# Performance work log

Measured on AMD Instinct MI355X. Metric: run time of the kernel, lower is better.

The kernel has to match this reference:

```python
import jax, jax.numpy as jnp
import numpy as np

N_NODES = 100000
DIM = 64
E_RAND = 1600000
NEG_SLOPE = 0.2


def setup_inputs() -> dict:
    key = jax.random.key(0)
    k = jax.random.split(key, 10)
    x = jax.random.normal(k[0], (N_NODES, DIM), dtype=jnp.float32)
    # random edges with src != dst, then append self-loops (PyG add_self_loops=True)
    src = jax.random.randint(k[1], (E_RAND,), 0, N_NODES)
    off = jax.random.randint(k[2], (E_RAND,), 1, N_NODES)
    dst = (src + off) % N_NODES
    loops = jnp.arange(N_NODES)
    edge_index = jnp.stack([jnp.concatenate([src, loops]),
                            jnp.concatenate([dst, loops])]).astype(jnp.int32)
    s = 1.0 / np.sqrt(DIM)  # ~glorot scale
    W_l = jax.random.normal(k[3], (DIM, DIM), dtype=jnp.float32) * s
    b_l = jnp.zeros((DIM,), dtype=jnp.float32)
    W_r = jax.random.normal(k[4], (DIM, DIM), dtype=jnp.float32) * s
    b_r = jnp.zeros((DIM,), dtype=jnp.float32)
    att = jax.random.normal(k[5], (DIM,), dtype=jnp.float32) * s
    bias = jnp.zeros((DIM,), dtype=jnp.float32)
    return {"x": x, "edge_index": edge_index, "W_l": W_l, "b_l": b_l,
            "W_r": W_r, "b_r": b_r, "att": att, "bias": bias}


def _gatv2_conv(x, src, dst, W_l, b_l, W_r, b_r, att, bias):
    # GATv2Conv, heads=1, concat=True, share_weights=False
    x_l = x @ W_l + b_l          # source/message transform  [N, D]
    x_r = x @ W_r + b_r          # target transform          [N, D]
    h = jax.nn.leaky_relu(x_l[src] + x_r[dst], NEG_SLOPE)  # [E, D]
    e = h @ att                  # per-edge score            [E]
    # scatter-softmax over incoming edges of each destination node
    m = jax.ops.segment_max(e, dst, num_segments=N_NODES)
    ex = jnp.exp(e - m[dst])
    denom = jax.ops.segment_sum(ex, dst, num_segments=N_NODES)
    alpha = ex / denom[dst]      # [E]
    out = jax.ops.segment_sum(alpha[:, None] * x_l[src], dst, num_segments=N_NODES)
    return out + bias


def reference(x, edge_index, W_l, b_l, W_r, b_r, att, bias):
    src, dst = edge_index[0], edge_index[1]
    h = _gatv2_conv(x, src, dst, W_l, b_l, W_r, b_r, att, bias)
    h = _gatv2_conv(h, src, dst, W_l, b_l, W_r, b_r, att, bias)
    return x + h  # residual=True
```

## Files before the change

kernel.cpp:

```cpp
#include <hip/hip_runtime.h>
#include <hip/hip_fp16.h>

#define DIMN 64
#define LROWS 128
#define XPAD 132
#define BK 256
#define NBMAX 512
#define P1E 8192
#define CAPB 6144

typedef _Float16 f16x2 __attribute__((ext_vector_type(2)));

__device__ __forceinline__ f16x2 asH2(unsigned u) {
  f16x2 r;
  __builtin_memcpy(&r, &u, 4);
  return r;
}
__device__ __forceinline__ unsigned asU(f16x2 h) {
  unsigned u;
  __builtin_memcpy(&u, &h, 4);
  return u;
}
__device__ __forceinline__ float4 cvt4u(uint2 u) {
  f16x2 a = asH2(u.x), b = asH2(u.y);
  return make_float4((float)a[0], (float)a[1], (float)b[0], (float)b[1]);
}
__device__ __forceinline__ uint2 pack4(float4 v) {
  f16x2 a = {(_Float16)v.x, (_Float16)v.y};
  f16x2 b = {(_Float16)v.z, (_Float16)v.w};
  uint2 u;
  u.x = asU(a);
  u.y = asU(b);
  return u;
}

template <bool IN_HALF>
__device__ __forceinline__ void linear_body(
    const void* __restrict__ xin,
    const float* __restrict__ Wl, const float* __restrict__ bl,
    const float* __restrict__ Wr, const float* __restrict__ br,
    __half* __restrict__ xlh, __half* __restrict__ xrh, int N, int bid,
    float* sWl, float* sWr, float* sxT)
{
  const float4* Wl4 = (const float4*)Wl;
  const float4* Wr4 = (const float4*)Wr;
  float4* sWl4 = (float4*)sWl;
  float4* sWr4 = (float4*)sWr;
  for (int i = threadIdx.x; i < DIMN * DIMN / 4; i += 256) {
    sWl4[i] = Wl4[i];
    sWr4[i] = Wr4[i];
  }
  int base = bid * LROWS;
  int nrows = min(LROWS, N - base);
  for (int i = threadIdx.x; i < LROWS * (DIMN / 4); i += 256) {
    int r = i >> 4;
    int k4 = (i & 15) * 4;
    float4 v = make_float4(0.f, 0.f, 0.f, 0.f);
    if (r < nrows) {
      if constexpr (IN_HALF)
        v = cvt4u(((const uint2*)xin)[(size_t)base * 16 + i]);
      else
        v = ((const float4*)xin)[(size_t)base * 16 + i];
    }
    sxT[(k4 + 0) * XPAD + r] = v.x;
    sxT[(k4 + 1) * XPAD + r] = v.y;
    sxT[(k4 + 2) * XPAD + r] = v.z;
    sxT[(k4 + 3) * XPAD + r] = v.w;
  }
  __syncthreads();

  int sub = threadIdx.x & 15;
  int dg = sub * 4;
  int rg = (threadIdx.x >> 4) * 8;
  float4 bl4 = *(const float4*)(bl + dg);
  float4 br4 = *(const float4*)(br + dg);
  float4 al[8], ar[8];
#pragma unroll
  for (int j = 0; j < 8; ++j) { al[j] = bl4; ar[j] = br4; }
#pragma unroll 2
  for (int k = 0; k < DIMN; ++k) {
    float4 wl = *(const float4*)(sWl + k * DIMN + dg);
    float4 wr = *(const float4*)(sWr + k * DIMN + dg);
    const float* xp = sxT + k * XPAD + rg;
    float4 xa = *(const float4*)(xp);
    float4 xb = *(const float4*)(xp + 4);
    float xs0 = xa.x, xs1 = xa.y, xs2 = xa.z, xs3 = xa.w;
    float xs4 = xb.x, xs5 = xb.y, xs6 = xb.z, xs7 = xb.w;
#define FMA_ROW(J, XV)                                              \
    al[J].x = fmaf(XV, wl.x, al[J].x);                              \
    al[J].y = fmaf(XV, wl.y, al[J].y);                              \
    al[J].z = fmaf(XV, wl.z, al[J].z);                              \
    al[J].w = fmaf(XV, wl.w, al[J].w);                              \
    ar[J].x = fmaf(XV, wr.x, ar[J].x);                              \
    ar[J].y = fmaf(XV, wr.y, ar[J].y);                              \
    ar[J].z = fmaf(XV, wr.z, ar[J].z);                              \
    ar[J].w = fmaf(XV, wr.w, ar[J].w);
    FMA_ROW(0, xs0) FMA_ROW(1, xs1) FMA_ROW(2, xs2) FMA_ROW(3, xs3)
    FMA_ROW(4, xs4) FMA_ROW(5, xs5) FMA_ROW(6, xs6) FMA_ROW(7, xs7)
#undef FMA_ROW
  }
#pragma unroll
  for (int j = 0; j < 8; ++j) {
    int r = base + rg + j;
    if (r < N) {
      ((uint2*)xlh)[(unsigned)r * 16u + sub] = pack4(al[j]);
      ((uint2*)xrh)[(unsigned)r * 16u + sub] = pack4(ar[j]);
    }
  }
}

__device__ __forceinline__ void p1_body(
    const int* __restrict__ src, const int* __restrict__ dst,
    int* __restrict__ bucketCnt, int* __restrict__ packed, int E,
    int bid, int* cnt, int* basea)
{
  for (int i = threadIdx.x; i < NBMAX; i += 256) cnt[i] = 0;
  __syncthreads();
  int e0 = bid * P1E;
  int e1 = min(e0 + P1E, E);
  for (int e = e0 + threadIdx.x; e < e1; e += 256)
    atomicAdd(&cnt[dst[e] >> 8], 1);
  __syncthreads();
  for (int b = threadIdx.x; b < NBMAX; b += 256) {
    int c = cnt[b];
    basea[b] = (c > 0) ? atomicAdd(&bucketCnt[b], c) : 0;
    cnt[b] = 0;
  }
  __syncthreads();
  for (int e = e0 + threadIdx.x; e < e1; e += 256) {
    int d = dst[e];
    int b = d >> 8;
    int pos = basea[b] + atomicAdd(&cnt[b], 1);
    if (pos < CAPB)
      packed[(size_t)b * CAPB + pos] = ((d & 255) << 24) | src[e];
  }
}

__global__ __launch_bounds__(256) void k_lin_p1(
    const float* __restrict__ x,
    const float* __restrict__ Wl, const float* __restrict__ bl,
    const float* __restrict__ Wr, const float* __restrict__ br,
    __half* __restrict__ xlh, __half* __restrict__ xrh, int N,
    const int* __restrict__ src, const int* __restrict__ dst,
    int* __restrict__ bucketCnt, int* __restrict__ packed, int E, int p1Grid)
{
  __shared__ __align__(16) float sWl[DIMN * DIMN];
  __shared__ __align__(16) float sWr[DIMN * DIMN];
  __shared__ __align__(16) float sxT[DIMN * XPAD];
  int bid = blockIdx.x;
  if (bid < p1Grid) {
    p1_body(src, dst, bucketCnt, packed, E, bid, (int*)sWl, (int*)sWr);
    return;
  }
  linear_body<false>(x, Wl, bl, Wr, br, xlh, xrh, N, bid - p1Grid,
                     sWl, sWr, sxT);
}

__global__ __launch_bounds__(256) void k_linear2(
    const __half* __restrict__ xin,
    const float* __restrict__ Wl, const float* __restrict__ bl,
    const float* __restrict__ Wr, const float* __restrict__ br,
    __half* __restrict__ xlh, __half* __restrict__ xrh, int N)
{
  __shared__ __align__(16) float sWl[DIMN * DIMN];
  __shared__ __align__(16) float sWr[DIMN * DIMN];
  __shared__ __align__(16) float sxT[DIMN * XPAD];
  linear_body<true>(xin, Wl, bl, Wr, br, xlh, xrh, N, blockIdx.x,
                    sWl, sWr, sxT);
}

__global__ __launch_bounds__(256) void k_p2(
    const int* __restrict__ packed, const int* __restrict__ bucketCnt,
    int* __restrict__ rowptr, int* __restrict__ deg,
    int* __restrict__ csr_src, int N)
{
  __shared__ int hist[BK];
  __shared__ int off[BK];
  __shared__ int cur[BK];
  int b = blockIdx.x;
  int t = threadIdx.x;
  int node0 = b * BK;
  int nn = min(BK, N - node0);
  hist[t] = 0;
  cur[t] = 0;
  __syncthreads();
  int cntB = min(bucketCnt[b], CAPB);
  const int* pk = packed + (size_t)b * CAPB;
  for (int i = t; i < cntB; i += 256)
    atomicAdd(&hist[(unsigned)pk[i] >> 24], 1);
  __syncthreads();
  int sz = (t < nn) ? ((hist[t] + 7) & ~7) : 0;
  off[t] = sz;
  __syncthreads();
  for (int s = 1; s < BK; s <<= 1) {
    int add = (t >= s) ? off[t - s] : 0;
    __syncthreads();
    off[t] += add;
    __syncthreads();
  }
  int aStart = (t == 0) ? 0 : off[t - 1];
  __syncthreads();
  off[t] = aStart;
  if (t < nn) {
    rowptr[node0 + t] = b * CAPB + aStart;
    deg[node0 + t] = hist[t];
  }
  __syncthreads();
  int* cb = csr_src + (size_t)b * CAPB;
  if (t < nn) {
    for (int z = aStart + hist[t]; z < aStart + sz; ++z) cb[z] = 0;
    if (t == nn - 1) {
      int e = aStart + sz;
      for (int k = 0; k < 24; ++k)
        if (e + k < CAPB) cb[e + k] = 0;
    }
  }
  __syncthreads();
  for (int i = t; i < cntB; i += 256) {
    int v = pk[i];
    int dl = (unsigned)v >> 24;
    int pos = off[dl] + atomicAdd(&cur[dl], 1);
    cb[pos] = (v & 0xFFFFFF) << 3;
  }
}

template <bool OUT_HALF>
__global__ __launch_bounds__(256) void k_node(
    const __half* __restrict__ xlh, const __half* __restrict__ xrh,
    const int* __restrict__ rowptr, const int* __restrict__ deg,
    const int* __restrict__ csr_src,
    const float* __restrict__ att, const float* __restrict__ bias,
    const float* __restrict__ resid, void* __restrict__ out, int N)
{
  int node = blockIdx.x * 4 + (threadIdx.x >> 6);
  int lane = threadIdx.x & 63;
  if (node >= N) return;
  int g = lane >> 3;
  int sub = lane & 7;
  int beg = rowptr[node];
  int cnt = deg[node];
  const int* cs = csr_src + beg;
  const uint4* xp = (const uint4*)xlh;

  uint4 ur = ((const uint4*)xrh)[(unsigned)node * 8u + sub];
  f16x2 xr0 = asH2(ur.x), xr1 = asH2(ur.y);
  f16x2 xr2 = asH2(ur.z), xr3 = asH2(ur.w);
  float4 ata = ((const float4*)att)[2 * sub];
  float4 atb = ((const float4*)att)[2 * sub + 1];
  f16x2 at0 = {(_Float16)ata.x, (_Float16)ata.y};
  f16x2 at1 = {(_Float16)ata.z, (_Float16)ata.w};
  f16x2 at2 = {(_Float16)atb.x, (_Float16)atb.y};
  f16x2 at3 = {(_Float16)atb.z, (_Float16)atb.w};
  const f16x2 k02 = {(_Float16)0.2f, (_Float16)0.2f};

  float den = 0.f;
  float4 ac0 = make_float4(0.f, 0.f, 0.f, 0.f);
  float4 ac1 = make_float4(0.f, 0.f, 0.f, 0.f);

  int niter = (cnt + 7) >> 3;
  uint4 ra = xp[(unsigned)cs[g] + sub];
  int q1 = (1 < niter) ? cs[8 + g] : 0;
  uint4 rb = xp[(unsigned)q1 + sub];
  int q2 = (2 < niter) ? cs[16 + g] : 0;

#define BODY(F, P_EXTRA)                                            \
    f16x2 x0 = asH2(F.x), x1 = asH2(F.y);                           \
    f16x2 x2 = asH2(F.z), x3 = asH2(F.w);                           \
    f16x2 s0 = x0 + xr0, s1 = x1 + xr1;                             \
    f16x2 s2 = x2 + xr2, s3 = x3 + xr3;                             \
    s0 = __builtin_elementwise_max(s0, s0 * k02);                   \
    s1 = __builtin_elementwise_max(s1, s1 * k02);                   \
    s2 = __builtin_elementwise_max(s2, s2 * k02);                   \
    s3 = __builtin_elementwise_max(s3, s3 * k02);                   \
    float wa = __builtin_amdgcn_fdot2(at0, s0, 0.f, false);         \
    float wb = __builtin_amdgcn_fdot2(at2, s2, 0.f, false);         \
    wa = __builtin_amdgcn_fdot2(at1, s1, wa, false);                \
    wb = __builtin_amdgcn_fdot2(at3, s3, wb, false);                \
    float w = wa + wb;                                              \
    w += __shfl_xor(w, 1);                                          \
    w += __shfl_xor(w, 2);                                          \
    w += __shfl_xor(w, 4);                                          \
    P_EXTRA                                                         \
    float p = __expf(w);                                            \
    den += p;                                                       \
    ac0.x = fmaf(p, (float)x0[0], ac0.x);                           \
    ac0.y = fmaf(p, (float)x0[1], ac0.y);                           \
    ac0.z = fmaf(p, (float)x1[0], ac0.z);                           \
    ac0.w = fmaf(p, (float)x1[1], ac0.w);                           \
    ac1.x = fmaf(p, (float)x2[0], ac1.x);                           \
    ac1.y = fmaf(p, (float)x2[1], ac1.y);                           \
    ac1.z = fmaf(p, (float)x3[0], ac1.z);                           \
    ac1.w = fmaf(p, (float)x3[1], ac1.w);

  int i = 0;
  for (; i < niter - 1; ++i) {
    uint4 rc = ra;
    if (i + 2 < niter) rc = xp[(unsigned)q2 + sub];
    int q3 = 0;
    if (i + 3 < niter) q3 = cs[((i + 3) << 3) + g];
    BODY(ra, )
    ra = rb; rb = rc; q2 = q3;
  }
  {
    BODY(ra, w = ((i << 3) + g < cnt) ? w : -INFINITY;)
  }
#undef BODY

  den += __shfl_xor(den, 8);
  den += __shfl_xor(den, 16);
  den += __shfl_xor(den, 32);
  bool l1 = (g & 1) == 0;
  float k0 = l1 ? ac0.x : ac1.x;
  float k1 = l1 ? ac0.y : ac1.y;
  float k2 = l1 ? ac0.z : ac1.z;
  float k3 = l1 ? ac0.w : ac1.w;
  k0 += __shfl_xor(l1 ? ac1.x : ac0.x, 8);
  k1 += __shfl_xor(l1 ? ac1.y : ac0.y, 8);
  k2 += __shfl_xor(l1 ? ac1.z : ac0.z, 8);
  k3 += __shfl_xor(l1 ? ac1.w : ac0.w, 8);
  bool l2 = (g & 2) == 0;
  float t0 = l2 ? k0 : k2;
  float t1 = l2 ? k1 : k3;
  t0 += __shfl_xor(l2 ? k2 : k0, 16);
  t1 += __shfl_xor(l2 ? k3 : k1, 16);
  bool l3 = (g & 4) == 0;
  float uk = l3 ? t0 : t1;
  uk += __shfl_xor(l3 ? t1 : t0, 32);
  int d = 8 * sub + (((g & 1) << 2) | (g & 2) | ((g & 4) >> 2));
  float inv = 1.0f / den;
  float o = fmaf(uk, inv, bias[d]);
  if constexpr (OUT_HALF) {
    ((_Float16*)out)[(unsigned)node * 64u + d] = (_Float16)o;
  } else {
    if (resid) o += resid[(unsigned)node * 64u + d];
    ((float*)out)[(unsigned)node * 64u + d] = o;
  }
}

extern "C" void kernel_launch(void* const* d_in, const int* in_sizes, int n_in,
                              void* d_out, int out_size, void* d_ws, size_t ws_size,
                              hipStream_t stream) {
  const float* x    = (const float*)d_in[0];
  const int*   ei   = (const int*)d_in[1];
  const float* W_l  = (const float*)d_in[2];
  const float* b_l  = (const float*)d_in[3];
  const float* W_r  = (const float*)d_in[4];
  const float* b_r  = (const float*)d_in[5];
  const float* att  = (const float*)d_in[6];
  const float* bias = (const float*)d_in[7];
  float* out = (float*)d_out;

  const int N = in_sizes[0] / DIMN;
  const int E = in_sizes[1] / 2;
  const int* src = ei;
  const int* dst = ei + E;
  const int nb = (N + BK - 1) / BK;

  __half* xlh = (__half*)d_ws;
  __half* xrh = xlh + (size_t)N * DIMN;
  __half* hh  = xrh + (size_t)N * DIMN;
  int* deg       = (int*)(hh + (size_t)N * DIMN);
  int* rowptr    = deg + N;
  int* bucketCnt = rowptr + N;
  int* csr_src   = bucketCnt + NBMAX;
  int* packed    = (int*)hh;

  const int linGrid  = (N + LROWS - 1) / LROWS;
  const int nodeGrid = (N + 3) / 4;
  const int p1Grid   = (E + P1E - 1) / P1E;

  hipMemsetAsync(bucketCnt, 0, (size_t)NBMAX * 4, stream);
  k_lin_p1<<<p1Grid + linGrid, 256, 0, stream>>>(
      x, W_l, b_l, W_r, b_r, xlh, xrh, N,
      src, dst, bucketCnt, packed, E, p1Grid);
  k_p2<<<nb, 256, 0, stream>>>(packed, bucketCnt, rowptr, deg, csr_src, N);

  k_node<true><<<nodeGrid, 256, 0, stream>>>(xlh, xrh, rowptr, deg, csr_src,
                                             att, bias, nullptr, hh, N);

  k_linear2<<<linGrid, 256, 0, stream>>>(hh, W_l, b_l, W_r, b_r,
                                         xlh, xrh, N);
  k_node<false><<<nodeGrid, 256, 0, stream>>>(xlh, xrh, rowptr, deg, csr_src,
                                              att, bias, x, out, N);
}
```

Before: 193.4 us.

## Stage bucketed edges in shared memory before coalesced scatter; split fused linear/p1 kernel

The edge-bucketing pass now computes a per-block prefix sum over bucket counts and stages each packed edge in shared memory, sorted by bucket. It then writes them out in bucket order, so global writes to the packed array become contiguous runs instead of scattered stores. The combined linear+p1 kernel is also split back into separate launches, which gives up the overlap between the two phases but lets the p1 kernel use its own larger shared-memory footprint. The added scan and extra barriers cost some latency per block, and one more kernel launch is added.

Result: slower. 219.7 us (+13.6%).

```diff
diff --git a/kernel.cpp b/kernel.cpp
--- a/kernel.cpp
+++ b/kernel.cpp
@@ -35,13 +35,15 @@
 }
 
 template <bool IN_HALF>
-__device__ __forceinline__ void linear_body(
+__global__ __launch_bounds__(256) void k_linear(
     const void* __restrict__ xin,
     const float* __restrict__ Wl, const float* __restrict__ bl,
     const float* __restrict__ Wr, const float* __restrict__ br,
-    __half* __restrict__ xlh, __half* __restrict__ xrh, int N, int bid,
-    float* sWl, float* sWr, float* sxT)
+    __half* __restrict__ xlh, __half* __restrict__ xrh, int N)
 {
+  __shared__ __align__(16) float sWl[DIMN * DIMN];
+  __shared__ __align__(16) float sWr[DIMN * DIMN];
+  __shared__ __align__(16) float sxT[DIMN * XPAD];
   const float4* Wl4 = (const float4*)Wl;
   const float4* Wr4 = (const float4*)Wr;
   float4* sWl4 = (float4*)sWl;
@@ -50,7 +52,7 @@
     sWl4[i] = Wl4[i];
     sWr4[i] = Wr4[i];
   }
-  int base = bid * LROWS;
+  int base = blockIdx.x * LROWS;
   int nrows = min(LROWS, N - base);
   for (int i = threadIdx.x; i < LROWS * (DIMN / 4); i += 256) {
     int r = i >> 4;
@@ -109,64 +111,58 @@
   }
 }
 
-__device__ __forceinline__ void p1_body(
+__global__ __launch_bounds__(256) void k_p1(
     const int* __restrict__ src, const int* __restrict__ dst,
-    int* __restrict__ bucketCnt, int* __restrict__ packed, int E,
-    int bid, int* cnt, int* basea)
+    int* __restrict__ bucketCnt, int* __restrict__ packed, int E)
 {
-  for (int i = threadIdx.x; i < NBMAX; i += 256) cnt[i] = 0;
-  __syncthreads();
-  int e0 = bid * P1E;
+  __shared__ int cnt[NBMAX];
+  __shared__ int runOff[NBMAX];
+  __shared__ int basea[NBMAX];
+  __shared__ int psum[256];
+  __shared__ int staged[P1E];
+  __shared__ unsigned short bkt[P1E];
+  int t = threadIdx.x;
+  cnt[t] = 0;
+  cnt[t + 256] = 0;
+  __syncthreads();
+  int e0 = blockIdx.x * P1E;
   int e1 = min(e0 + P1E, E);
-  for (int e = e0 + threadIdx.x; e < e1; e += 256)
+  int nE = e1 - e0;
+  for (int e = e0 + t; e < e1; e += 256)
     atomicAdd(&cnt[dst[e] >> 8], 1);
   __syncthreads();
-  for (int b = threadIdx.x; b < NBMAX; b += 256) {
-    int c = cnt[b];
-    basea[b] = (c > 0) ? atomicAdd(&bucketCnt[b], c) : 0;
-    cnt[b] = 0;
-  }
-  __syncthreads();
-  for (int e = e0 + threadIdx.x; e < e1; e += 256) {
+  int a0 = cnt[2 * t], a1 = cnt[2 * t + 1];
+  psum[t] = a0 + a1;
+  __syncthreads();
+  for (int s = 1; s < 256; s <<= 1) {
+    int add = (t >= s) ? psum[t - s] : 0;
+    __syncthreads();
+    psum[t] += add;
+    __syncthreads();
+  }
+  int excl = (t == 0) ? 0 : psum[t - 1];
+  runOff[2 * t] = excl;
+  runOff[2 * t + 1] = excl + a0;
+  basea[2 * t]     = a0 > 0 ? atomicAdd(&bucketCnt[2 * t], a0) : 0;
+  basea[2 * t + 1] = a1 > 0 ? atomicAdd(&bucketCnt[2 * t + 1], a1) : 0;
+  __syncthreads();
+  cnt[t] = 0;
+  cnt[t + 256] = 0;
+  __syncthreads();
+  for (int e = e0 + t; e < e1; e += 256) {
     int d = dst[e];
     int b = d >> 8;
-    int pos = basea[b] + atomicAdd(&cnt[b], 1);
-    if (pos < CAPB)
-      packed[(size_t)b * CAPB + pos] = ((d & 255) << 24) | src[e];
-  }
-}
-
-__global__ __launch_bounds__(256) void k_lin_p1(
-    const float* __restrict__ x,
-    const float* __restrict__ Wl, const float* __restrict__ bl,
-    const float* __restrict__ Wr, const float* __restrict__ br,
-    __half* __restrict__ xlh, __half* __restrict__ xrh, int N,
-    const int* __restrict__ src, const int* __restrict__ dst,
-    int* __restrict__ bucketCnt, int* __restrict__ packed, int E, int p1Grid)
-{
-  __shared__ __align__(16) float sWl[DIMN * DIMN];
-  __shared__ __align__(16) float sWr[DIMN * DIMN];
-  __shared__ __align__(16) float sxT[DIMN * XPAD];
-  int bid = blockIdx.x;
-  if (bid < p1Grid) {
-    p1_body(src, dst, bucketCnt, packed, E, bid, (int*)sWl, (int*)sWr);
-    return;
-  }
-  linear_body<false>(x, Wl, bl, Wr, br, xlh, xrh, N, bid - p1Grid,
-                     sWl, sWr, sxT);
-}
-
-__global__ __launch_bounds__(256) void k_linear2(
-    const __half* __restrict__ xin,
-    const float* __restrict__ Wl, const float* __restrict__ bl,
-    const float* __restrict__ Wr, const float* __restrict__ br,
-    __half* __restrict__ xlh, __half* __restrict__ xrh, int N)
-{
-  __shared__ __align__(16) float sWl[DIMN * DIMN];
-  __shared__ __align__(16) float sWr[DIMN * DIMN];
-  __shared__ __align__(16) float sxT[DIMN * XPAD];
-  linear_body<true>(xin, Wl, bl, Wr, br, xlh, xrh, N, blockIdx.x,
-                    sWl, sWr, sxT);
+    int pos = runOff[b] + atomicAdd(&cnt[b], 1);
+    staged[pos] = ((d & 255) << 24) | src[e];
+    bkt[pos] = (unsigned short)b;
+  }
+  __syncthreads();
+  for (int i = t; i < nE; i += 256) {
+    int b = bkt[i];
+    int slot = basea[b] + (i - runOff[b]);
+    if (slot < CAPB)
+      packed[(size_t)b * CAPB + slot] = staged[i];
+  }
 }
 
 __global__ __launch_bounds__(256) void k_p2(
@@ -370,16 +366,16 @@
   const int p1Grid   = (E + P1E - 1) / P1E;
 
   hipMemsetAsync(bucketCnt, 0, (size_t)NBMAX * 4, stream);
-  k_lin_p1<<<p1Grid + linGrid, 256, 0, stream>>>(
-      x, W_l, b_l, W_r, b_r, xlh, xrh, N,
-      src, dst, bucketCnt, packed, E, p1Grid);
+  k_p1<<<p1Grid, 256, 0, stream>>>(src, dst, bucketCnt, packed, E);
   k_p2<<<nb, 256, 0, stream>>>(packed, bucketCnt, rowptr, deg, csr_src, N);
 
+  k_linear<false><<<linGrid, 256, 0, stream>>>(x, W_l, b_l, W_r, b_r,
+                                               xlh, xrh, N);
   k_node<true><<<nodeGrid, 256, 0, stream>>>(xlh, xrh, rowptr, deg, csr_src,
                                              att, bias, nullptr, hh, N);
 
-  k_linear2<<<linGrid, 256, 0, stream>>>(hh, W_l, b_l, W_r, b_r,
-                                         xlh, xrh, N);
+  k_linear<true><<<linGrid, 256, 0, stream>>>(hh, W_l, b_l, W_r, b_r,
+                                              xlh, xrh, N);
   k_node<false><<<nodeGrid, 256, 0, stream>>>(xlh, xrh, rowptr, deg, csr_src,
                                               att, bias, x, out, N);
 }
```
